# Performance work log

Hardware: AMD Instinct MI355X
Metric: run time of the kernel (lower is better)

Reference implementation:

```python
import jax, jax.numpy as jnp
import numpy as np

POS_SCALE = 50.0
LEN_SCALE = 500.0

N_NODES = 100000
N_EDGES = 600000
IN_DIM = 128
HID_DIM = 128


def setup_inputs() -> dict:
    key = jax.random.key(0)
    ks = jax.random.split(key, 12)
    x = jax.random.normal(ks[0], (N_NODES, IN_DIM), dtype=jnp.float32)
    positions = jax.random.randint(ks[1], (N_NODES,), 0, 50, dtype=jnp.int64)
    lengths = jax.random.randint(ks[2], (N_NODES,), 0, 500, dtype=jnp.int64)
    edge_index = jax.random.randint(ks[3], (2, N_EDGES), 0, N_NODES, dtype=jnp.int64)
    reranker_scores = jax.random.normal(ks[4], (N_NODES,), dtype=jnp.float32)
    s = 1.0 / np.sqrt(IN_DIM + 2)
    fp_w = jax.random.uniform(ks[5], (IN_DIM + 2, IN_DIM), minval=-s, maxval=s, dtype=jnp.float32)
    fp_b = jnp.zeros((IN_DIM,), jnp.float32)
    s2 = 1.0 / np.sqrt(IN_DIM)
    lin_l_w = jax.random.uniform(ks[6], (IN_DIM, HID_DIM), minval=-s2, maxval=s2, dtype=jnp.float32)
    lin_l_b = jnp.zeros((HID_DIM,), jnp.float32)
    lin_r_w = jax.random.uniform(ks[7], (IN_DIM, HID_DIM), minval=-s2, maxval=s2, dtype=jnp.float32)
    res_w = jax.random.uniform(ks[8], (IN_DIM, HID_DIM), minval=-s2, maxval=s2, dtype=jnp.float32)
    res_b = jnp.zeros((HID_DIM,), jnp.float32)
    s3 = 1.0 / np.sqrt(HID_DIM)
    sh_w = jax.random.uniform(ks[9], (HID_DIM, 1), minval=-s3, maxval=s3, dtype=jnp.float32)
    sh_b = jnp.zeros((1,), jnp.float32)
    alpha = jnp.asarray(0.65, jnp.float32)
    return {
        "x": x, "positions": positions, "lengths": lengths,
        "edge_index": edge_index, "reranker_scores": reranker_scores,
        "fp_w": fp_w, "fp_b": fp_b,
        "lin_l_w": lin_l_w, "lin_l_b": lin_l_b, "lin_r_w": lin_r_w,
        "res_w": res_w, "res_b": res_b,
        "sh_w": sh_w, "sh_b": sh_b, "alpha": alpha,
    }


def reference(x, positions, lengths, edge_index, reranker_scores,
              fp_w, fp_b, lin_l_w, lin_l_b, lin_r_w, res_w, res_b,
              sh_w, sh_b, alpha):
    n = x.shape[0]
    # position/length features
    pos_feat = positions[:, None].astype(x.dtype) / POS_SCALE
    len_feat = lengths[:, None].astype(x.dtype) / LEN_SCALE
    xf = jnp.concatenate([x, pos_feat, len_feat], axis=-1)  # [N, D+2]
    xf = xf @ fp_w + fp_b                                   # [N, D]
    h_in = xf @ res_w + res_b                               # residual proj [N, H]
    # SAGEConv with mean aggregation: out = lin_l(mean_{j->i} x_j) + lin_r(x_i)
    src, dst = edge_index[0], edge_index[1]
    msg_sum = jax.ops.segment_sum(xf[src], dst, num_segments=n)          # [N, D]
    cnt = jax.ops.segment_sum(jnp.ones((src.shape[0], 1), xf.dtype), dst, num_segments=n)
    agg = msg_sum / jnp.maximum(cnt, 1.0)
    h = jax.nn.relu(agg @ lin_l_w + lin_l_b + xf @ lin_r_w)  # [N, H]
    # dropout is identity in eval mode
    h = h + h_in
    gnn_scores = (h @ sh_w + sh_b)[:, 0]                     # [N]
    a = jax.nn.sigmoid(alpha)
    return a * reranker_scores + (1.0 - a) * gnn_scores
```

## Files before the change

kernel.cpp:

```cpp
#include <hip/hip_runtime.h>
#include <hip/hip_bf16.h>
#include <cstdint>

#define D 128
#define LDSPITCH 136
#define LB 64
#define DCAP 32
#define NBLK 64
#define NBMAX 2048

typedef __attribute__((ext_vector_type(4))) float f32x4;
typedef __attribute__((ext_vector_type(8))) short s16x8;

__device__ __forceinline__ unsigned short f2b(float f) {
    union { float f; uint32_t u; } v; v.f = f;
    uint32_t b = v.u + 0x7fffu + ((v.u >> 16) & 1u);
    return (unsigned short)(b >> 16);
}
__device__ __forceinline__ float b2f(unsigned short u) {
    union { uint32_t u; float f; } v; v.u = ((uint32_t)u) << 16; return v.f;
}

__global__ __launch_bounds__(256) void k_prep(
    const float* __restrict__ fp_w, const float* __restrict__ lin_l_w,
    const float* __restrict__ lin_r_w,
    unsigned short* __restrict__ Btf, unsigned short* __restrict__ Btl,
    unsigned short* __restrict__ Btr,
    const float* __restrict__ res_w, const float* __restrict__ res_b,
    const float* __restrict__ sh_w, const float* __restrict__ sh_b,
    const float* __restrict__ alpha, float* __restrict__ c1, float* __restrict__ scal,
    const int* __restrict__ ei, int* __restrict__ histg, int E, int EBLK, int NB) {
    __shared__ int h[NBMAX];
    int bid = blockIdx.x, tid = threadIdx.x;
    if (bid < 192) {
        int m = bid >> 6;
        int i = (bid & 63) * 256 + tid;
        const float* src = (m == 0) ? fp_w : (m == 1) ? lin_l_w : lin_r_w;
        unsigned short* dst = (m == 0) ? Btf : (m == 1) ? Btl : Btr;
        int k = i >> 7, n = i & 127;
        dst[n * D + k] = f2b(src[k * D + n]);
    } else if (bid == 192) {
        if (tid < 128) {
            float s = 0.f;
            for (int j = 0; j < D; ++j) s += res_w[tid * D + j] * sh_w[j];
            c1[tid] = s;
            if (tid == 0) {
                float c0 = 0.f;
                for (int j = 0; j < D; ++j) c0 += res_b[j] * sh_w[j];
                c0 += sh_b[0];
                float a = 1.f / (1.f + expf(-alpha[0]));
                scal[0] = a; scal[1] = c0;
            }
        }
    } else {
        int k = bid - 193;
        for (int j = tid; j < NB; j += 256) h[j] = 0;
        __syncthreads();
        int s = k * EBLK, e = s + EBLK; if (e > E) e = E;
        for (int i = s + tid; i < e; i += 256)
            atomicAdd(&h[ei[E + i] >> 6], 1);
        __syncthreads();
        for (int j = tid; j < NB; j += 256) histg[j * NBLK + k] = h[j];
    }
}

__global__ __launch_bounds__(256) void k_scan1(
    int* __restrict__ histg, int* __restrict__ total, int NB) {
    int b = blockIdx.x * 256 + threadIdx.x;
    if (b >= NB) return;
    int* p = histg + (size_t)b * NBLK;
    int run = 0;
#pragma unroll 8
    for (int k = 0; k < NBLK; ++k) { int t = p[k]; p[k] = run; run += t; }
    total[b] = run;
}

__global__ __launch_bounds__(256) void k_scan2(
    const int* __restrict__ total, int* __restrict__ base, int NB) {
    __shared__ int sh[256];
    int tid = threadIdx.x;
    int carry = 0;
    int nch = (NB + 255) >> 8;
    for (int c = 0; c < nch; ++c) {
        int idx = c * 256 + tid;
        int v = idx < NB ? total[idx] : 0;
        sh[tid] = v;
        __syncthreads();
        for (int off = 1; off < 256; off <<= 1) {
            int u = (tid >= off) ? sh[tid - off] : 0;
            __syncthreads();
            if (tid >= off) sh[tid] += u;
            __syncthreads();
        }
        if (idx < NB) base[idx] = carry + sh[tid] - v;
        int chtot = sh[255];
        __syncthreads();
        carry += chtot;
    }
    if (tid == 0) base[NB] = carry;
}

__global__ __launch_bounds__(256) void k_gemm1(
    const float* __restrict__ x, unsigned short* __restrict__ xb,
    const int* __restrict__ positions, const int* __restrict__ lengths,
    const unsigned short* __restrict__ Btf,
    const float* __restrict__ fp_w, const float* __restrict__ fp_b,
    const float* __restrict__ c1, float* __restrict__ d1, int N, int mb,
    const int* __restrict__ ei, const int* __restrict__ histg,
    const int* __restrict__ base, int* __restrict__ coarse, int E, int EBLK, int NB) {
    __shared__ int cur[NBMAX];
    if (blockIdx.x >= mb) {
        int tid = threadIdx.x;
        int k = blockIdx.x - mb;
        for (int j = tid; j < NB; j += 256)
            cur[j] = base[j] + histg[(size_t)j * NBLK + k];
        __syncthreads();
        int s = k * EBLK, e = s + EBLK; if (e > E) e = E;
        for (int i = s + tid; i < e; i += 256) {
            int sv = ei[i];
            int d  = ei[E + i];
            int p = atomicAdd(&cur[d >> 6], 1);
            coarse[p] = sv | ((d & 63) << 17);
        }
        return;
    }
    int lane = threadIdx.x & 63;
    int wv = threadIdx.x >> 6;
    int col = lane & 15, q = lane >> 4;
    int row0 = blockIdx.x * 64 + wv * 16;
    int arow = row0 + col; if (arow > N - 1) arow = N - 1;

    f32x4 acc[8];
#pragma unroll
    for (int nt = 0; nt < 8; ++nt) acc[nt] = (f32x4){0.f, 0.f, 0.f, 0.f};

#pragma unroll
    for (int ks = 0; ks < 4; ++ks) {
        const float* xp = x + (size_t)arow * D + ks * 32 + q * 8;
        float4 a0 = *(const float4*)xp;
        float4 a1 = *(const float4*)(xp + 4);
        s16x8 af;
        af[0] = (short)f2b(a0.x); af[1] = (short)f2b(a0.y);
        af[2] = (short)f2b(a0.z); af[3] = (short)f2b(a0.w);
        af[4] = (short)f2b(a1.x); af[5] = (short)f2b(a1.y);
        af[6] = (short)f2b(a1.z); af[7] = (short)f2b(a1.w);
#pragma unroll
        for (int nt = 0; nt < 8; ++nt) {
            s16x8 bf = *(const s16x8*)(Btf + (size_t)(nt * 16 + col) * D + ks * 32 + q * 8);
            acc[nt] = __builtin_amdgcn_mfma_f32_16x16x32_bf16(af, bf, acc[nt], 0, 0, 0);
        }
    }

    float pf[4], lf[4];
#pragma unroll
    for (int r = 0; r < 4; ++r) {
        int rr = row0 + q * 4 + r; int rc = rr < N ? rr : N - 1;
        pf[r] = (float)positions[rc] * (1.0f / 50.0f);
        lf[r] = (float)lengths[rc] * (1.0f / 500.0f);
    }
    float sdot[4] = {0.f, 0.f, 0.f, 0.f};
#pragma unroll
    for (int nt = 0; nt < 8; ++nt) {
        int n = nt * 16 + col;
        float bias = fp_b[n];
        float w128 = fp_w[128 * D + n];
        float w129 = fp_w[129 * D + n];
        float c1v = c1[n];
#pragma unroll
        for (int r = 0; r < 4; ++r) {
            float t = acc[nt][r] + bias + pf[r] * w128 + lf[r] * w129;
            int rr = row0 + q * 4 + r;
            if (rr < N) xb[(size_t)rr * D + n] = f2b(t);
            sdot[r] += t * c1v;
        }
    }
#pragma unroll
    for (int r = 0; r < 4; ++r) {
        float s = sdot[r];
        s += __shfl_xor(s, 1, 64);
        s += __shfl_xor(s, 2, 64);
        s += __shfl_xor(s, 4, 64);
        s += __shfl_xor(s, 8, 64);
        if (col == 0) {
            int rr = row0 + q * 4 + r;
            if (rr < N) d1[rr] = s;
        }
    }
}

__global__ __launch_bounds__(256) void k_gemm2(
    const unsigned short* __restrict__ xfb,
    const int* __restrict__ base, const int* __restrict__ coarse,
    const unsigned short* __restrict__ Btl, const unsigned short* __restrict__ Btr,
    const float* __restrict__ lin_l_b, const float* __restrict__ sh_w,
    const float* __restrict__ rer, const float* __restrict__ d1,
    const float* __restrict__ scal, float* __restrict__ out, int N) {
    __shared__ unsigned short agg[64 * LDSPITCH];
    __shared__ int dense[64][DCAP];
    __shared__ int cnt64[64];
    int tid = threadIdx.x;
    int lane = tid & 63;
    int wv = tid >> 6;
    int li = lane & 15, q = lane >> 4;
    int wrow0 = blockIdx.x * 64 + wv * 16;
    int Nm1 = N - 1;

    int arow = wrow0 + li; if (arow > Nm1) arow = Nm1;
    s16x8 afx[4];
#pragma unroll
    for (int ks = 0; ks < 4; ++ks)
        afx[ks] = *(const s16x8*)(xfb + (size_t)arow * D + ks * 32 + q * 8);

    int b0 = base[blockIdx.x], cnt = base[blockIdx.x + 1] - b0;
    if (tid < 64) cnt64[tid] = 0;
    __syncthreads();
    for (int i = tid; i < cnt; i += 256) {
        int v = coarse[b0 + i];
        int l = v >> 17;
        int p = atomicAdd(&cnt64[l], 1);
        if (p < DCAP) dense[l][p] = v & 0x1ffff;
    }
    __syncthreads();

    float t[4][8];
#pragma unroll
    for (int rr = 0; rr < 4; ++rr)
#pragma unroll
        for (int k2 = 0; k2 < 8; ++k2) t[rr][k2] = 0.f;

    int dgq[4];
#pragma unroll
    for (int rr = 0; rr < 4; ++rr) {
        int dg = cnt64[wv * 16 + rr * 4 + q];
        dgq[rr] = dg > DCAP ? DCAP : dg;
    }

#pragma unroll
    for (int rr = 0; rr < 4; ++rr) {
        int dg = dgq[rr];
        const int* dr = &dense[wv * 16 + rr * 4 + q][0];
        int4 ja = *(const int4*)dr;
        int4 jb = *(const int4*)(dr + 4);
        int ix[8] = {ja.x, ja.y, ja.z, ja.w, jb.x, jb.y, jb.z, jb.w};
        s16x8 v[8];
#pragma unroll
        for (int k = 0; k < 8; ++k) {
            int c = ix[k];
            c = c > 0 ? c : 0;
            c = c < Nm1 ? c : Nm1;
            v[k] = *(const s16x8*)(xfb + (size_t)c * D + li * 8);
        }
        float w[8];
#pragma unroll
        for (int k = 0; k < 8; ++k) w[k] = (k < dg) ? 1.f : 0.f;
#pragma unroll
        for (int k = 0; k < 8; ++k)
#pragma unroll
            for (int k2 = 0; k2 < 8; ++k2)
                t[rr][k2] += w[k] * b2f((unsigned short)v[k][k2]);
    }

#pragma unroll
    for (int rr = 0; rr < 4; ++rr) {
        int dg = dgq[rr];
        if (dg > 8) {
            const int* dr = &dense[wv * 16 + rr * 4 + q][0];
            for (int j = 8; j < dg; j += 8) {
                int4 jc = *(const int4*)(dr + j);
                int4 jd = *(const int4*)(dr + j + 4);
                int ix[8] = {jc.x, jc.y, jc.z, jc.w, jd.x, jd.y, jd.z, jd.w};
                s16x8 v[8];
#pragma unroll
                for (int k = 0; k < 8; ++k) {
                    int c = ix[k];
                    c = c > 0 ? c : 0;
                    c = c < Nm1 ? c : Nm1;
                    v[k] = *(const s16x8*)(xfb + (size_t)c * D + li * 8);
                }
                float w[8];
#pragma unroll
                for (int k = 0; k < 8; ++k) w[k] = (j + k < dg) ? 1.f : 0.f;
#pragma unroll
                for (int k = 0; k < 8; ++k)
#pragma unroll
                    for (int k2 = 0; k2 < 8; ++k2)
                        t[rr][k2] += w[k] * b2f((unsigned short)v[k][k2]);
            }
        }
    }

#pragma unroll
    for (int rr = 0; rr < 4; ++rr) {
        int dg = dgq[rr];
        float rc = 1.0f / (float)(dg > 0 ? dg : 1);
        s16x8 o;
#pragma unroll
        for (int k2 = 0; k2 < 8; ++k2) o[k2] = (short)f2b(t[rr][k2] * rc);
        *(s16x8*)(agg + (wv * 16 + rr * 4 + q) * LDSPITCH + li * 8) = o;
    }

    f32x4 acc[8];
#pragma unroll
    for (int nt = 0; nt < 8; ++nt) acc[nt] = (f32x4){0.f, 0.f, 0.f, 0.f};

#pragma unroll
    for (int ks = 0; ks < 4; ++ks) {
        s16x8 afa = *(const s16x8*)(agg + (wv * 16 + li) * LDSPITCH + ks * 32 + q * 8);
        s16x8 bfl[8];
#pragma unroll
        for (int nt = 0; nt < 8; ++nt)
            bfl[nt] = *(const s16x8*)(Btl + (size_t)(nt * 16 + li) * D + ks * 32 + q * 8);
#pragma unroll
        for (int nt = 0; nt < 8; ++nt)
            acc[nt] = __builtin_amdgcn_mfma_f32_16x16x32_bf16(afa, bfl[nt], acc[nt], 0, 0, 0);
        s16x8 bfr[8];
#pragma unroll
        for (int nt = 0; nt < 8; ++nt)
            bfr[nt] = *(const s16x8*)(Btr + (size_t)(nt * 16 + li) * D + ks * 32 + q * 8);
#pragma unroll
        for (int nt = 0; nt < 8; ++nt)
            acc[nt] = __builtin_amdgcn_mfma_f32_16x16x32_bf16(afx[ks], bfr[nt], acc[nt], 0, 0, 0);
    }

    float a = scal[0], c0 = scal[1];
    float sdot[4] = {0.f, 0.f, 0.f, 0.f};
#pragma unroll
    for (int nt = 0; nt < 8; ++nt) {
        int n = nt * 16 + li;
        float bias = lin_l_b[n];
        float shw = sh_w[n];
#pragma unroll
        for (int r = 0; r < 4; ++r) {
            float tt = acc[nt][r] + bias;
            sdot[r] += fmaxf(tt, 0.f) * shw;
        }
    }
#pragma unroll
    for (int r = 0; r < 4; ++r) {
        float s = sdot[r];
        s += __shfl_xor(s, 1, 64);
        s += __shfl_xor(s, 2, 64);
        s += __shfl_xor(s, 4, 64);
        s += __shfl_xor(s, 8, 64);
        if (li == 0) {
            int rr = wrow0 + q * 4 + r;
            if (rr < N) out[rr] = a * rer[rr] + (1.f - a) * (c0 + d1[rr] + s);
        }
    }
}

extern "C" void kernel_launch(void* const* d_in, const int* in_sizes, int n_in,
                              void* d_out, int out_size, void* d_ws, size_t ws_size,
                              hipStream_t stream) {
    const float* x        = (const float*)d_in[0];
    const int*   positions= (const int*)d_in[1];
    const int*   lengths  = (const int*)d_in[2];
    const int*   ei       = (const int*)d_in[3];
    const float* rer      = (const float*)d_in[4];
    const float* fp_w     = (const float*)d_in[5];
    const float* fp_b     = (const float*)d_in[6];
    const float* lin_l_w  = (const float*)d_in[7];
    const float* lin_l_b  = (const float*)d_in[8];
    const float* lin_r_w  = (const float*)d_in[9];
    const float* res_w    = (const float*)d_in[10];
    const float* res_b    = (const float*)d_in[11];
    const float* sh_w     = (const float*)d_in[12];
    const float* sh_b     = (const float*)d_in[13];
    const float* alpha    = (const float*)d_in[14];
    int N = in_sizes[1];
    int E = in_sizes[3] / 2;
    float* out = (float*)d_out;

    int NB = (N + LB - 1) / LB;
    int EBLK = (E + NBLK - 1) / NBLK;
    int mb = (N + 63) / 64;

    char* ws = (char*)d_ws;
    size_t off = 0;
    auto alloc = [&](size_t bytes) -> void* {
        void* p = ws + off;
        off = (off + bytes + 255) & ~(size_t)255;
        return p;
    };
    unsigned short* xb  = (unsigned short*)alloc((size_t)N * D * 2);
    int* coarse  = (int*)alloc(((size_t)E + 64) * 4);
    int* histg   = (int*)alloc((size_t)NB * NBLK * 4);
    int* total   = (int*)alloc((size_t)NB * 4);
    int* base    = (int*)alloc(((size_t)NB + 1) * 4);
    float* d1    = (float*)alloc((size_t)N * 4);
    unsigned short* Btf = (unsigned short*)alloc(D * D * 2);
    unsigned short* Btl = (unsigned short*)alloc(D * D * 2);
    unsigned short* Btr = (unsigned short*)alloc(D * D * 2);
    float* c1    = (float*)alloc(D * 4);
    float* scal  = (float*)alloc(16);

    k_prep<<<193 + NBLK, 256, 0, stream>>>(fp_w, lin_l_w, lin_r_w, Btf, Btl, Btr,
                                           res_w, res_b, sh_w, sh_b, alpha, c1, scal,
                                           ei, histg, E, EBLK, NB);
    k_scan1<<<(NB + 255) / 256, 256, 0, stream>>>(histg, total, NB);
    k_scan2<<<1, 256, 0, stream>>>(total, base, NB);
    k_gemm1<<<mb + NBLK, 256, 0, stream>>>(x, xb, positions, lengths, Btf, fp_w, fp_b,
                                           c1, d1, N, mb, ei, histg, base, coarse,
                                           E, EBLK, NB);
    k_gemm2<<<mb, 256, 0, stream>>>(xb, base, coarse, Btl, Btr, lin_l_b, sh_w,
                                    rer, d1, scal, out, N);
}
```

Before: 261.0 us.

## Fold histogram scan kernels into the scatter blocks of gemm1

Removes the two separate scan kernel launches (k_scan1, k_scan2). Each scatter block in k_gemm1 now reads all 64 per-block histograms, computes its own exclusive offsets and the global bucket prefix sum in shared memory, and block 0 writes base. The histogram layout becomes block-major so these reads coalesce. This cuts two launches and their serialization, but every scatter block repeats the full histogram reduction and scan, about 64x2048 reads per block, which could delay the scatter.

```diff
diff --git a/kernel.cpp b/kernel.cpp
--- a/kernel.cpp
+++ b/kernel.cpp
@@ -8,6 +8,7 @@
 #define DCAP 32
 #define NBLK 64
 #define NBMAX 2048
+#define NBS 2048
 
 typedef __attribute__((ext_vector_type(4))) float f32x4;
 typedef __attribute__((ext_vector_type(8))) short s16x8;
@@ -60,44 +61,8 @@
         for (int i = s + tid; i < e; i += 256)
             atomicAdd(&h[ei[E + i] >> 6], 1);
         __syncthreads();
-        for (int j = tid; j < NB; j += 256) histg[j * NBLK + k] = h[j];
-    }
-}
-
-__global__ __launch_bounds__(256) void k_scan1(
-    int* __restrict__ histg, int* __restrict__ total, int NB) {
-    int b = blockIdx.x * 256 + threadIdx.x;
-    if (b >= NB) return;
-    int* p = histg + (size_t)b * NBLK;
-    int run = 0;
-#pragma unroll 8
-    for (int k = 0; k < NBLK; ++k) { int t = p[k]; p[k] = run; run += t; }
-    total[b] = run;
-}
-
-__global__ __launch_bounds__(256) void k_scan2(
-    const int* __restrict__ total, int* __restrict__ base, int NB) {
-    __shared__ int sh[256];
-    int tid = threadIdx.x;
-    int carry = 0;
-    int nch = (NB + 255) >> 8;
-    for (int c = 0; c < nch; ++c) {
-        int idx = c * 256 + tid;
-        int v = idx < NB ? total[idx] : 0;
-        sh[tid] = v;
-        __syncthreads();
-        for (int off = 1; off < 256; off <<= 1) {
-            int u = (tid >= off) ? sh[tid - off] : 0;
-            __syncthreads();
-            if (tid >= off) sh[tid] += u;
-            __syncthreads();
-        }
-        if (idx < NB) base[idx] = carry + sh[tid] - v;
-        int chtot = sh[255];
-        __syncthreads();
-        carry += chtot;
-    }
-    if (tid == 0) base[NB] = carry;
+        for (int j = tid; j < NB; j += 256) histg[(size_t)k * NBS + j] = h[j];
+    }
 }
 
 __global__ __launch_bounds__(256) void k_gemm1(
@@ -107,16 +72,48 @@
     const float* __restrict__ fp_w, const float* __restrict__ fp_b,
     const float* __restrict__ c1, float* __restrict__ d1, int N, int mb,
     const int* __restrict__ ei, const int* __restrict__ histg,
-    const int* __restrict__ base, int* __restrict__ coarse, int E, int EBLK, int NB) {
+    int* __restrict__ base, int* __restrict__ coarse, int E, int EBLK, int NB) {
     __shared__ int cur[NBMAX];
+    __shared__ int totl[NBMAX];
+    __shared__ int part[256];
     if (blockIdx.x >= mb) {
         int tid = threadIdx.x;
         int k = blockIdx.x - mb;
-        for (int j = tid; j < NB; j += 256)
-            cur[j] = base[j] + histg[(size_t)j * NBLK + k];
-        __syncthreads();
-        int s = k * EBLK, e = s + EBLK; if (e > E) e = E;
-        for (int i = s + tid; i < e; i += 256) {
+        for (int j = tid; j < NB; j += 256) { cur[j] = 0; totl[j] = 0; }
+        __syncthreads();
+        for (int kk = 0; kk < NBLK; ++kk) {
+            const int* hp = histg + (size_t)kk * NBS;
+            bool addc = kk < k;
+            for (int j = tid; j < NB; j += 256) {
+                int v = hp[j];
+                totl[j] += v;
+                if (addc) cur[j] += v;
+            }
+        }
+        __syncthreads();
+        int C = (NB + 255) >> 8;
+        int j0 = tid * C; if (j0 > NB) j0 = NB;
+        int j1 = j0 + C;  if (j1 > NB) j1 = NB;
+        int s = 0;
+        for (int j = j0; j < j1; ++j) { int v = totl[j]; totl[j] = s; s += v; }
+        part[tid] = s;
+        __syncthreads();
+        for (int off = 1; off < 256; off <<= 1) {
+            int u = (tid >= off) ? part[tid - off] : 0;
+            __syncthreads();
+            if (tid >= off) part[tid] += u;
+            __syncthreads();
+        }
+        int pex = part[tid] - s;
+        for (int j = j0; j < j1; ++j) {
+            int b = totl[j] + pex;
+            cur[j] += b;
+            if (k == 0) base[j] = b;
+        }
+        if (k == 0 && tid == 0) base[NB] = part[255];
+        __syncthreads();
+        int s_ = k * EBLK, e_ = s_ + EBLK; if (e_ > E) e_ = E;
+        for (int i = s_ + tid; i < e_; i += 256) {
             int sv = ei[i];
             int d  = ei[E + i];
             int p = atomicAdd(&cur[d >> 6], 1);
@@ -384,8 +381,7 @@
     };
     unsigned short* xb  = (unsigned short*)alloc((size_t)N * D * 2);
     int* coarse  = (int*)alloc(((size_t)E + 64) * 4);
-    int* histg   = (int*)alloc((size_t)NB * NBLK * 4);
-    int* total   = (int*)alloc((size_t)NB * 4);
+    int* histg   = (int*)alloc((size_t)NBLK * NBS * 4);
     int* base    = (int*)alloc(((size_t)NB + 1) * 4);
     float* d1    = (float*)alloc((size_t)N * 4);
     unsigned short* Btf = (unsigned short*)alloc(D * D * 2);
@@ -397,8 +393,6 @@
     k_prep<<<193 + NBLK, 256, 0, stream>>>(fp_w, lin_l_w, lin_r_w, Btf, Btl, Btr,
                                            res_w, res_b, sh_w, sh_b, alpha, c1, scal,
                                            ei, histg, E, EBLK, NB);
-    k_scan1<<<(NB + 255) / 256, 256, 0, stream>>>(histg, total, NB);
-    k_scan2<<<1, 256, 0, stream>>>(total, base, NB);
     k_gemm1<<<mb + NBLK, 256, 0, stream>>>(x, xb, positions, lengths, Btf, fp_w, fp_b,
                                            c1, d1, N, mb, ei, histg, base, coarse,
                                            E, EBLK, NB);
```

After: 361.7 us. +38.6%, slower.
